# Kernel tuning notes

Measured on AMD Instinct MI355X. Metric: run time of the kernel, lower is better.

Reference implementation:

```python
import jax, jax.numpy as jnp
import numpy as np

EPS = 0.05  # blend weight of K_Rectify smoothing


def k_rectify(x_nbc, distance, idx, eps=EPS):
    """Distance-weighted neighbor smoothing.
    x_nbc: (N, B, C); distance, idx: (B, N, K). Returns (N, B, C)."""
    x_bnc = jnp.transpose(x_nbc, (1, 0, 2))                       # (B,N,C)
    B = x_bnc.shape[0]
    neigh = x_bnc[jnp.arange(B)[:, None, None], idx]              # (B,N,K,C) gather
    w = jax.nn.softmax(-distance, axis=-1)                        # closer -> larger weight
    smoothed = jnp.einsum('bnk,bnkc->bnc', w, neigh)              # (B,N,C)
    y = (1.0 - eps) * x_bnc + eps * smoothed
    return jnp.transpose(y, (1, 0, 2))


def monarch_linear(x, w1, w2, bias):
    """Monarch block-diagonal butterfly multiply on the last dim.
    w1: (k,q,p), w2: (l,s,r) with k*p == n, l*r == k*q."""
    shp = x.shape
    k, q, p = w1.shape
    l, s, r = w2.shape
    xb = x.reshape(-1, k, p)
    o1 = jnp.einsum('kqp,bkp->bkq', w1, xb)                       # (B*, k, q)
    o1 = o1.reshape(-1, r, l).transpose(0, 2, 1)                  # 'b (r l) -> b l r'
    o2 = jnp.einsum('lsr,blr->bls', w2, o1)                       # (B*, l, s)
    out = o2.transpose(0, 2, 1).reshape(-1, s * l) + bias         # 'b l s -> b (s l)'
    return out.reshape(*shp[:-1], s * l)


def setup_inputs() -> dict:
    key = jax.random.key(0)
    B, N, C, K, nblocks = 8, 8192, 256, 8, 8
    blk = C // nblocks
    ks = jax.random.split(key, 6)
    x = jax.random.normal(ks[0], (B, N, C), dtype=jnp.float32)
    distance = jax.random.uniform(ks[1], (B, N, K), dtype=jnp.float32)
    idx = jax.random.randint(ks[2], (B, N, K), 0, N)
    rf = jax.random.normal(ks[3], (B, N, C), dtype=jnp.float32)
    scale = 1.0 / np.sqrt(blk)
    w1 = jax.random.normal(ks[4], (nblocks, blk, blk), dtype=jnp.float32) * scale
    w2 = jax.random.normal(ks[5], (nblocks, blk, blk), dtype=jnp.float32) * scale
    bias = jnp.zeros((C,), dtype=jnp.float32)
    return {"x": x, "distance": distance, "idx": idx, "rf": rf,
            "w1": w1, "w2": w2, "bias": bias}


def reference(x, distance, idx, rf, w1, w2, bias):
    # _prepare_in: (B,N,C) -> (N,B,C)
    xs = jnp.transpose(x, (1, 0, 2))
    s1 = k_rectify(xs, distance, idx)            # smooth_in
    t = monarch_linear(s1, w1, w2, bias)         # Monarch block-diag matmul
    s2 = k_rectify(t, distance, idx)             # smooth_out
    return jnp.transpose(s2, (1, 0, 2)) + rf     # _out_transform residual
```

## Files before the change

kernel.cpp:

```cpp
#include <hip/hip_runtime.h>

#define NPTS 8192
#define CH   256
#define KNB  8
#define NROWS 65536
#define ROWS_PER_BLK 32
#define PHASE_ROWS 16
#define FT_STRIDE 36

#define NBLK_CONV 8192
#define NBLK_S1   (NROWS / ROWS_PER_BLK)
#define NBLK_S2   (NROWS / 16)

typedef unsigned short ushort_t;
typedef float  f32x4  __attribute__((ext_vector_type(4)));

#define BARRIER_LDS() do { \
    asm volatile("s_waitcnt lgkmcnt(0)" ::: "memory"); \
    __builtin_amdgcn_s_barrier(); \
} while (0)

__device__ __forceinline__ int xcd_swz(int h, int cpx) {
    return (h & 7) * cpx + (h >> 3);
}

__device__ __forceinline__ ushort_t f32_to_bf16(float f) {
    unsigned int b = __float_as_uint(f);
    b += 0x7FFFu + ((b >> 16) & 1u);
    return (ushort_t)(b >> 16);
}
__device__ __forceinline__ float bf16_to_f32(ushort_t u) {
    return __uint_as_float(((unsigned int)u) << 16);
}
__device__ __forceinline__ unsigned int pack_bf16(float lo, float hi) {
    return (unsigned int)f32_to_bf16(lo) | ((unsigned int)f32_to_bf16(hi) << 16);
}
__device__ __forceinline__ f32x4 bf4(ushort4 u) {
    f32x4 r;
    r.x = bf16_to_f32(u.x); r.y = bf16_to_f32(u.y);
    r.z = bf16_to_f32(u.z); r.w = bf16_to_f32(u.w);
    return r;
}

__global__ __launch_bounds__(256) void pm_conv(
    const f32x4* __restrict__ x, uint4* __restrict__ xb)
{
    const int l = xcd_swz(blockIdx.x, NBLK_CONV / 8);
    const size_t i = (size_t)l * 256 + threadIdx.x;
    const f32x4 a = __builtin_nontemporal_load(&x[2 * i]);
    const f32x4 c = __builtin_nontemporal_load(&x[2 * i + 1]);
    uint4 o;
    o.x = pack_bf16(a.x, a.y);
    o.y = pack_bf16(a.z, a.w);
    o.z = pack_bf16(c.x, c.y);
    o.w = pack_bf16(c.z, c.w);
    xb[i] = o;
}

__global__ __launch_bounds__(256, 4) void pm_stage1(
    const ushort_t* __restrict__ xb, const float* __restrict__ dist,
    const int* __restrict__ idx, const float* __restrict__ w1,
    const float* __restrict__ w2, const float* __restrict__ bias,
    ushort_t* __restrict__ t)
{
    const int c = threadIdx.x;

    __shared__ float s1[PHASE_ROWS][CH];
    __shared__ float fT[PHASE_ROWS][8 * FT_STRIDE];

    const float bb = bias[c];
    const int l2   = c & 7;
    const int kb   = c >> 5;
    const int ftw  = l2 * FT_STRIDE + (c >> 3);

    const int rr   = __builtin_amdgcn_readfirstlane(threadIdx.x >> 6);
    const int lane = threadIdx.x & 63;

    const int lb       = xcd_swz(blockIdx.x, NBLK_S1 / 8);
    const int row_base = lb * ROWS_PER_BLK;
    const int b = row_base >> 13;
    const char* xbase  = (const char*)(xb + (size_t)b * NPTS * CH);
    const int laneoff  = lane * 8;

#define LOAD_META(dd, nn, row) do {                                        \
    const float4 m0_ = *(const float4*)(dist + (size_t)(row) * KNB);       \
    const float4 m1_ = *(const float4*)(dist + (size_t)(row) * KNB + 4);   \
    const int4   j0_ = *(const int4*)(idx + (size_t)(row) * KNB);          \
    const int4   j1_ = *(const int4*)(idx + (size_t)(row) * KNB + 4);      \
    dd[0]=m0_.x; dd[1]=m0_.y; dd[2]=m0_.z; dd[3]=m0_.w;                    \
    dd[4]=m1_.x; dd[5]=m1_.y; dd[6]=m1_.z; dd[7]=m1_.w;                    \
    nn[0]=__builtin_amdgcn_readfirstlane(j0_.x);                           \
    nn[1]=__builtin_amdgcn_readfirstlane(j0_.y);                           \
    nn[2]=__builtin_amdgcn_readfirstlane(j0_.z);                           \
    nn[3]=__builtin_amdgcn_readfirstlane(j0_.w);                           \
    nn[4]=__builtin_amdgcn_readfirstlane(j1_.x);                           \
    nn[5]=__builtin_amdgcn_readfirstlane(j1_.y);                           \
    nn[6]=__builtin_amdgcn_readfirstlane(j1_.z);                           \
    nn[7]=__builtin_amdgcn_readfirstlane(j1_.w);                           \
} while (0)

#define ISSUE_G(cc, gg, nn, row) do {                                      \
    const int rloc_ = (row) & (NPTS - 1);                                  \
    cc = *(const ushort4*)(xbase + ((size_t)rloc_ << 9) + laneoff);        \
    _Pragma("unroll")                                                      \
    for (int k_ = 0; k_ < KNB; ++k_)                                       \
        gg[k_] = *(const ushort4*)(xbase + ((size_t)(unsigned)nn[k_] << 9) + laneoff); \
} while (0)

#define BLEND(cc, gg, dd, srow) do {                                       \
    float mn_ = dd[0];                                                     \
    _Pragma("unroll")                                                      \
    for (int k_ = 1; k_ < KNB; ++k_) mn_ = fminf(mn_, dd[k_]);             \
    float e_[KNB]; float sum_ = 0.f;                                       \
    _Pragma("unroll")                                                      \
    for (int k_ = 0; k_ < KNB; ++k_) { e_[k_] = __expf(mn_ - dd[k_]); sum_ += e_[k_]; } \
    const float inv_ = 0.05f / sum_;                                       \
    f32x4 acc_ = 0.95f * bf4(cc);                                          \
    _Pragma("unroll")                                                      \
    for (int k_ = 0; k_ < KNB; ++k_) acc_ += (e_[k_] * inv_) * bf4(gg[k_]); \
    *(f32x4*)(&s1[srow][lane * 4]) = acc_;                                 \
} while (0)

    float dA[KNB], dB[KNB];
    int   nA[KNB], nB[KNB];
    ushort4 cA, gA[KNB], cB, gB[KNB];

    LOAD_META(dA, nA, row_base + rr);
    LOAD_META(dB, nB, row_base + 4 + rr);
    ISSUE_G(cA, gA, nA, row_base + rr);
    ISSUE_G(cB, gB, nB, row_base + 4 + rr);

#pragma unroll
    for (int ph = 0; ph < 2; ++ph) {
        const int prow = row_base + ph * PHASE_ROWS + rr;

        BLEND(cA, gA, dA, 0 * 4 + rr);
        LOAD_META(dA, nA, prow + 8);  ISSUE_G(cA, gA, nA, prow + 8);
        BLEND(cB, gB, dB, 1 * 4 + rr);
        LOAD_META(dB, nB, prow + 12); ISSUE_G(cB, gB, nB, prow + 12);
        BLEND(cA, gA, dA, 2 * 4 + rr);
        BLEND(cB, gB, dB, 3 * 4 + rr);

        BARRIER_LDS();

        f32x4 w1r[8];
        {
            const f32x4* w1p = (const f32x4*)(w1 + c * 32);
#pragma unroll
            for (int i = 0; i < 8; ++i) { w1r[i] = w1p[i]; asm volatile("" : "+v"(w1r[i])); }
        }
#pragma unroll
        for (int r2 = 0; r2 < PHASE_ROWS; ++r2) {
            const f32x4* sb = (const f32x4*)(&s1[r2][kb * 32]);
            f32x4 a4 = {0.f, 0.f, 0.f, 0.f};
#pragma unroll
            for (int p4 = 0; p4 < 8; ++p4) a4 += w1r[p4] * sb[p4];
            fT[r2][ftw] = (a4.x + a4.y) + (a4.z + a4.w);
        }

        if (ph == 0) {
            LOAD_META(dA, nA, row_base + PHASE_ROWS + rr);
            ISSUE_G(cA, gA, nA, row_base + PHASE_ROWS + rr);
            LOAD_META(dB, nB, row_base + PHASE_ROWS + 4 + rr);
            ISSUE_G(cB, gB, nB, row_base + PHASE_ROWS + 4 + rr);
        }

        BARRIER_LDS();

        f32x4 w2r[8];
        {
            const f32x4* w2p = (const f32x4*)(w2 + ((c & 7) * 32 + (c >> 3)) * 32);
#pragma unroll
            for (int i = 0; i < 8; ++i) { w2r[i] = w2p[i]; asm volatile("" : "+v"(w2r[i])); }
        }
#pragma unroll
        for (int r2 = 0; r2 < PHASE_ROWS; ++r2) {
            const f32x4* fp = (const f32x4*)(&fT[r2][l2 * FT_STRIDE]);
            f32x4 a4 = {0.f, 0.f, 0.f, 0.f};
#pragma unroll
            for (int r4 = 0; r4 < 8; ++r4) a4 += w2r[r4] * fp[r4];
            const float a = bb + ((a4.x + a4.y) + (a4.z + a4.w));
            __builtin_nontemporal_store(
                f32_to_bf16(a),
                &t[(size_t)(row_base + ph * PHASE_ROWS + r2) * CH + c]);
        }
    }
#undef LOAD_META
#undef ISSUE_G
#undef BLEND
}

__global__ __launch_bounds__(256, 4) void pm_stage2(
    const ushort_t* __restrict__ t, const float* __restrict__ dist,
    const int* __restrict__ idx, const float* __restrict__ rf,
    float* __restrict__ out)
{
    const int w     = __builtin_amdgcn_readfirstlane(threadIdx.x >> 6);
    const int lane  = threadIdx.x & 63;
    const int lb    = xcd_swz(blockIdx.x, NBLK_S2 / 8);
    const int wrow0 = lb * 16 + w * 4;
    const int b     = wrow0 >> 13;
    const char* tbase = (const char*)(t + (size_t)b * NPTS * CH);
    const int laneoff = lane * 8;

    int   nbs[4][KNB];
    float d [4][KNB];
#pragma unroll
    for (int r = 0; r < 4; ++r) {
        const int row = wrow0 + r;
        const float4 d0 = *(const float4*)(dist + (size_t)row * KNB);
        const float4 d1 = *(const float4*)(dist + (size_t)row * KNB + 4);
        const int4   i0 = *(const int4*)(idx + (size_t)row * KNB);
        const int4   i1 = *(const int4*)(idx + (size_t)row * KNB + 4);
        d[r][0]=d0.x; d[r][1]=d0.y; d[r][2]=d0.z; d[r][3]=d0.w;
        d[r][4]=d1.x; d[r][5]=d1.y; d[r][6]=d1.z; d[r][7]=d1.w;
        nbs[r][0]=__builtin_amdgcn_readfirstlane(i0.x);
        nbs[r][1]=__builtin_amdgcn_readfirstlane(i0.y);
        nbs[r][2]=__builtin_amdgcn_readfirstlane(i0.z);
        nbs[r][3]=__builtin_amdgcn_readfirstlane(i0.w);
        nbs[r][4]=__builtin_amdgcn_readfirstlane(i1.x);
        nbs[r][5]=__builtin_amdgcn_readfirstlane(i1.y);
        nbs[r][6]=__builtin_amdgcn_readfirstlane(i1.z);
        nbs[r][7]=__builtin_amdgcn_readfirstlane(i1.w);
    }

    ushort4 c0[4], g[4][KNB];
    f32x4   rv[4];
#pragma unroll
    for (int r = 0; r < 4; ++r) {
        const int rloc = (wrow0 + r) & (NPTS - 1);
        c0[r] = *(const ushort4*)(tbase + ((size_t)rloc << 9) + laneoff);
        rv[r] = __builtin_nontemporal_load(
                    &((const f32x4*)rf)[(size_t)(wrow0 + r) * 64 + lane]);
#pragma unroll
        for (int k = 0; k < KNB; ++k)
            g[r][k] = *(const ushort4*)(tbase + ((size_t)(unsigned)nbs[r][k] << 9) + laneoff);
    }

#pragma unroll
    for (int r = 0; r < 4; ++r) {
        float mn = d[r][0];
#pragma unroll
        for (int k = 1; k < KNB; ++k) mn = fminf(mn, d[r][k]);
        float e[KNB]; float sum = 0.f;
#pragma unroll
        for (int k = 0; k < KNB; ++k) { e[k] = __expf(mn - d[r][k]); sum += e[k]; }
        const float inv = 0.05f / sum;

        f32x4 acc = 0.95f * bf4(c0[r]) + rv[r];
#pragma unroll
        for (int k = 0; k < KNB; ++k)
            acc += (e[k] * inv) * bf4(g[r][k]);
        __builtin_nontemporal_store(
            acc, &((f32x4*)out)[(size_t)(wrow0 + r) * 64 + lane]);
    }
}

extern "C" void kernel_launch(void* const* d_in, const int* in_sizes, int n_in,
                              void* d_out, int out_size, void* d_ws, size_t ws_size,
                              hipStream_t stream) {
    const float* x    = (const float*)d_in[0];
    const float* dist = (const float*)d_in[1];
    const int*   idx  = (const int*)d_in[2];
    const float* rf   = (const float*)d_in[3];
    const float* w1   = (const float*)d_in[4];
    const float* w2   = (const float*)d_in[5];
    const float* bias = (const float*)d_in[6];
    float* out = (float*)d_out;

    ushort_t* t  = (ushort_t*)d_ws;
    ushort_t* xb = (ushort_t*)((char*)d_ws + (size_t)NROWS * CH * 2);

    pm_conv  <<<NBLK_CONV, 256, 0, stream>>>((const f32x4*)x, (uint4*)xb);
    pm_stage1<<<NBLK_S1,   256, 0, stream>>>(xb, dist, idx, w1, w2, bias, t);
    pm_stage2<<<NBLK_S2,   256, 0, stream>>>(t, dist, idx, rf, out);
}
```

Before: 280.7 us.

## Use bf16 MFMA for Monarch block matmuls in stage1 with swizzled LDS

Stage 1 now blends all 32 rows first and stores the smoothed rows as bf16 in XOR-swizzled LDS. It then runs both Monarch block-diagonal multiplies with 16x16x32 bf16 MFMA instructions instead of scalar fp32 FMAs over fp32 LDS, with the weights converted to bf16 on the fly. The intermediate result and the final output are staged through LDS so the global store of t is coalesced. This adds bf16 rounding of the weights and the intermediate (a precision loss) and replaces the two-phase overlap of gathers and compute with a single pass.

After: 236.6 us. 1.19x faster.

```diff
diff --git a/kernel.cpp b/kernel.cpp
--- a/kernel.cpp
+++ b/kernel.cpp
@@ -4,16 +4,18 @@
 #define CH   256
 #define KNB  8
 #define NROWS 65536
-#define ROWS_PER_BLK 32
-#define PHASE_ROWS 16
-#define FT_STRIDE 36
-
+#define RPB_S1 32
 #define NBLK_CONV 8192
-#define NBLK_S1   (NROWS / ROWS_PER_BLK)
+#define NBLK_S1   (NROWS / RPB_S1)
 #define NBLK_S2   (NROWS / 16)
+
+#define S1_STRIDE 544
+#define FS_STRIDE 656
+#define FS_L      80
 
 typedef unsigned short ushort_t;
 typedef float  f32x4  __attribute__((ext_vector_type(4)));
+typedef short  bf16x8 __attribute__((ext_vector_type(8)));
 
 #define BARRIER_LDS() do { \
     asm volatile("s_waitcnt lgkmcnt(0)" ::: "memory"); \
@@ -35,11 +37,18 @@
 __device__ __forceinline__ unsigned int pack_bf16(float lo, float hi) {
     return (unsigned int)f32_to_bf16(lo) | ((unsigned int)f32_to_bf16(hi) << 16);
 }
-__device__ __forceinline__ f32x4 bf4(ushort4 u) {
-    f32x4 r;
-    r.x = bf16_to_f32(u.x); r.y = bf16_to_f32(u.y);
-    r.z = bf16_to_f32(u.z); r.w = bf16_to_f32(u.w);
+__device__ __forceinline__ bf16x8 pack8w(const float* __restrict__ p) {
+    bf16x8 r;
+#pragma unroll
+    for (int j = 0; j < 8; ++j) r[j] = (short)f32_to_bf16(p[j]);
     return r;
+}
+
+__device__ __forceinline__ unsigned char* s1addr(unsigned char* base, int row, int byte_off) {
+    return base + row * S1_STRIDE + (byte_off ^ ((row & 7) << 4));
+}
+__device__ __forceinline__ unsigned char* fsaddr(unsigned char* base, int row, int byte_off) {
+    return base + row * FS_STRIDE + (byte_off ^ ((row & 7) << 4));
 }
 
 __global__ __launch_bounds__(256) void pm_conv(
@@ -63,22 +72,15 @@
     const float* __restrict__ w2, const float* __restrict__ bias,
     ushort_t* __restrict__ t)
 {
-    const int c = threadIdx.x;
-
-    __shared__ float s1[PHASE_ROWS][CH];
-    __shared__ float fT[PHASE_ROWS][8 * FT_STRIDE];
-
-    const float bb = bias[c];
-    const int l2   = c & 7;
-    const int kb   = c >> 5;
-    const int ftw  = l2 * FT_STRIDE + (c >> 3);
-
-    const int rr   = __builtin_amdgcn_readfirstlane(threadIdx.x >> 6);
     const int lane = threadIdx.x & 63;
+    const int wv   = __builtin_amdgcn_readfirstlane(threadIdx.x >> 6);
+
+    __shared__ __align__(16) unsigned char s1b[RPB_S1 * S1_STRIDE];
+    __shared__ __align__(16) unsigned char fsb[RPB_S1 * FS_STRIDE];
 
     const int lb       = xcd_swz(blockIdx.x, NBLK_S1 / 8);
-    const int row_base = lb * ROWS_PER_BLK;
-    const int b = row_base >> 13;
+    const int row_base = lb * RPB_S1;
+    const int b        = row_base >> 13;
     const char* xbase  = (const char*)(xb + (size_t)b * NPTS * CH);
     const int laneoff  = lane * 8;
 
@@ -107,7 +109,7 @@
         gg[k_] = *(const ushort4*)(xbase + ((size_t)(unsigned)nn[k_] << 9) + laneoff); \
 } while (0)
 
-#define BLEND(cc, gg, dd, srow) do {                                       \
+#define BLEND_W(cc, gg, dd, rl_) do {                                      \
     float mn_ = dd[0];                                                     \
     _Pragma("unroll")                                                      \
     for (int k_ = 1; k_ < KNB; ++k_) mn_ = fminf(mn_, dd[k_]);             \
@@ -115,79 +117,167 @@
     _Pragma("unroll")                                                      \
     for (int k_ = 0; k_ < KNB; ++k_) { e_[k_] = __expf(mn_ - dd[k_]); sum_ += e_[k_]; } \
     const float inv_ = 0.05f / sum_;                                       \
-    f32x4 acc_ = 0.95f * bf4(cc);                                          \
+    float ax_ = 0.95f * bf16_to_f32(cc.x);                                 \
+    float ay_ = 0.95f * bf16_to_f32(cc.y);                                 \
+    float az_ = 0.95f * bf16_to_f32(cc.z);                                 \
+    float aw_ = 0.95f * bf16_to_f32(cc.w);                                 \
     _Pragma("unroll")                                                      \
-    for (int k_ = 0; k_ < KNB; ++k_) acc_ += (e_[k_] * inv_) * bf4(gg[k_]); \
-    *(f32x4*)(&s1[srow][lane * 4]) = acc_;                                 \
+    for (int k_ = 0; k_ < KNB; ++k_) {                                     \
+        const float w_ = e_[k_] * inv_;                                    \
+        ax_ += w_ * bf16_to_f32(gg[k_].x);                                 \
+        ay_ += w_ * bf16_to_f32(gg[k_].y);                                 \
+        az_ += w_ * bf16_to_f32(gg[k_].z);                                 \
+        aw_ += w_ * bf16_to_f32(gg[k_].w);                                 \
+    }                                                                      \
+    uint2 pv_;                                                             \
+    pv_.x = pack_bf16(ax_, ay_);                                           \
+    pv_.y = pack_bf16(az_, aw_);                                           \
+    *(uint2*)s1addr(s1b, rl_, lane * 8) = pv_;                             \
 } while (0)
 
     float dA[KNB], dB[KNB];
     int   nA[KNB], nB[KNB];
     ushort4 cA, gA[KNB], cB, gB[KNB];
 
-    LOAD_META(dA, nA, row_base + rr);
-    LOAD_META(dB, nB, row_base + 4 + rr);
-    ISSUE_G(cA, gA, nA, row_base + rr);
-    ISSUE_G(cB, gB, nB, row_base + 4 + rr);
-
-#pragma unroll
-    for (int ph = 0; ph < 2; ++ph) {
-        const int prow = row_base + ph * PHASE_ROWS + rr;
-
-        BLEND(cA, gA, dA, 0 * 4 + rr);
-        LOAD_META(dA, nA, prow + 8);  ISSUE_G(cA, gA, nA, prow + 8);
-        BLEND(cB, gB, dB, 1 * 4 + rr);
-        LOAD_META(dB, nB, prow + 12); ISSUE_G(cB, gB, nB, prow + 12);
-        BLEND(cA, gA, dA, 2 * 4 + rr);
-        BLEND(cB, gB, dB, 3 * 4 + rr);
-
-        BARRIER_LDS();
-
-        f32x4 w1r[8];
-        {
-            const f32x4* w1p = (const f32x4*)(w1 + c * 32);
-#pragma unroll
-            for (int i = 0; i < 8; ++i) { w1r[i] = w1p[i]; asm volatile("" : "+v"(w1r[i])); }
-        }
-#pragma unroll
-        for (int r2 = 0; r2 < PHASE_ROWS; ++r2) {
-            const f32x4* sb = (const f32x4*)(&s1[r2][kb * 32]);
-            f32x4 a4 = {0.f, 0.f, 0.f, 0.f};
-#pragma unroll
-            for (int p4 = 0; p4 < 8; ++p4) a4 += w1r[p4] * sb[p4];
-            fT[r2][ftw] = (a4.x + a4.y) + (a4.z + a4.w);
-        }
-
-        if (ph == 0) {
-            LOAD_META(dA, nA, row_base + PHASE_ROWS + rr);
-            ISSUE_G(cA, gA, nA, row_base + PHASE_ROWS + rr);
-            LOAD_META(dB, nB, row_base + PHASE_ROWS + 4 + rr);
-            ISSUE_G(cB, gB, nB, row_base + PHASE_ROWS + 4 + rr);
-        }
-
-        BARRIER_LDS();
-
-        f32x4 w2r[8];
-        {
-            const f32x4* w2p = (const f32x4*)(w2 + ((c & 7) * 32 + (c >> 3)) * 32);
-#pragma unroll
-            for (int i = 0; i < 8; ++i) { w2r[i] = w2p[i]; asm volatile("" : "+v"(w2r[i])); }
-        }
-#pragma unroll
-        for (int r2 = 0; r2 < PHASE_ROWS; ++r2) {
-            const f32x4* fp = (const f32x4*)(&fT[r2][l2 * FT_STRIDE]);
-            f32x4 a4 = {0.f, 0.f, 0.f, 0.f};
-#pragma unroll
-            for (int r4 = 0; r4 < 8; ++r4) a4 += w2r[r4] * fp[r4];
-            const float a = bb + ((a4.x + a4.y) + (a4.z + a4.w));
-            __builtin_nontemporal_store(
-                f32_to_bf16(a),
-                &t[(size_t)(row_base + ph * PHASE_ROWS + r2) * CH + c]);
+    LOAD_META(dA, nA, row_base + wv);
+    LOAD_META(dB, nB, row_base + 4 + wv);
+    ISSUE_G(cA, gA, nA, row_base + wv);
+    ISSUE_G(cB, gB, nB, row_base + 4 + wv);
+
+#pragma unroll
+    for (int p = 0; p < 8; ++p) {
+        const int rl   = p * 4 + wv;
+        const int rown = row_base + (p + 2) * 4 + wv;
+
+        float4 dn0, dn1; int4 in0, in1;
+        if (p < 6) {
+            dn0 = *(const float4*)(dist + (size_t)rown * KNB);
+            dn1 = *(const float4*)(dist + (size_t)rown * KNB + 4);
+            in0 = *(const int4*)(idx + (size_t)rown * KNB);
+            in1 = *(const int4*)(idx + (size_t)rown * KNB + 4);
+        }
+
+        if ((p & 1) == 0) {
+            BLEND_W(cA, gA, dA, rl);
+            if (p < 6) {
+                dA[0]=dn0.x; dA[1]=dn0.y; dA[2]=dn0.z; dA[3]=dn0.w;
+                dA[4]=dn1.x; dA[5]=dn1.y; dA[6]=dn1.z; dA[7]=dn1.w;
+                nA[0]=__builtin_amdgcn_readfirstlane(in0.x);
+                nA[1]=__builtin_amdgcn_readfirstlane(in0.y);
+                nA[2]=__builtin_amdgcn_readfirstlane(in0.z);
+                nA[3]=__builtin_amdgcn_readfirstlane(in0.w);
+                nA[4]=__builtin_amdgcn_readfirstlane(in1.x);
+                nA[5]=__builtin_amdgcn_readfirstlane(in1.y);
+                nA[6]=__builtin_amdgcn_readfirstlane(in1.z);
+                nA[7]=__builtin_amdgcn_readfirstlane(in1.w);
+                ISSUE_G(cA, gA, nA, rown);
+            }
+        } else {
+            BLEND_W(cB, gB, dB, rl);
+            if (p < 6) {
+                dB[0]=dn0.x; dB[1]=dn0.y; dB[2]=dn0.z; dB[3]=dn0.w;
+                dB[4]=dn1.x; dB[5]=dn1.y; dB[6]=dn1.z; dB[7]=dn1.w;
+                nB[0]=__builtin_amdgcn_readfirstlane(in0.x);
+                nB[1]=__builtin_amdgcn_readfirstlane(in0.y);
+                nB[2]=__builtin_amdgcn_readfirstlane(in0.z);
+                nB[3]=__builtin_amdgcn_readfirstlane(in0.w);
+                nB[4]=__builtin_amdgcn_readfirstlane(in1.x);
+                nB[5]=__builtin_amdgcn_readfirstlane(in1.y);
+                nB[6]=__builtin_amdgcn_readfirstlane(in1.z);
+                nB[7]=__builtin_amdgcn_readfirstlane(in1.w);
+                ISSUE_G(cB, gB, nB, rown);
+            }
         }
     }
 #undef LOAD_META
 #undef ISSUE_G
-#undef BLEND
+#undef BLEND_W
+
+    BARRIER_LDS();
+
+    const int l15 = lane & 15;
+    const int kq  = lane >> 4;
+#pragma unroll
+    for (int kk = 0; kk < 2; ++kk) {
+        const int kb = wv * 2 + kk;
+        const int ao = kb * 64 + kq * 16;
+        const bf16x8 a0 = *(const bf16x8*)s1addr(s1b, l15, ao);
+        const bf16x8 a1 = *(const bf16x8*)s1addr(s1b, 16 + l15, ao);
+        const bf16x8 b0 = pack8w(w1 + (size_t)(kb * 32 + l15) * 32 + kq * 8);
+        const bf16x8 b1 = pack8w(w1 + (size_t)(kb * 32 + 16 + l15) * 32 + kq * 8);
+        f32x4 d00 = {0.f,0.f,0.f,0.f}, d01 = d00, d10 = d00, d11 = d00;
+        d00 = __builtin_amdgcn_mfma_f32_16x16x32_bf16(a0, b0, d00, 0, 0, 0);
+        d01 = __builtin_amdgcn_mfma_f32_16x16x32_bf16(a0, b1, d01, 0, 0, 0);
+        d10 = __builtin_amdgcn_mfma_f32_16x16x32_bf16(a1, b0, d10, 0, 0, 0);
+        d11 = __builtin_amdgcn_mfma_f32_16x16x32_bf16(a1, b1, d11, 0, 0, 0);
+#pragma unroll
+        for (int nt = 0; nt < 2; ++nt) {
+            const int qq = nt * 16 + l15;
+            const int fo = (qq & 7) * FS_L + (kb * 4 + (qq >> 3)) * 2;
+#pragma unroll
+            for (int mt = 0; mt < 2; ++mt) {
+                const f32x4 dd = (mt == 0) ? (nt == 0 ? d00 : d01)
+                                           : (nt == 0 ? d10 : d11);
+#pragma unroll
+                for (int reg = 0; reg < 4; ++reg) {
+                    const int row = mt * 16 + kq * 4 + reg;
+                    *(ushort_t*)fsaddr(fsb, row, fo) = f32_to_bf16(dd[reg]);
+                }
+            }
+        }
+    }
+
+    BARRIER_LDS();
+
+    {
+        const int l20 = wv * 2;
+        const bf16x8 fa00 = *(const bf16x8*)fsaddr(fsb, l15,      l20 * FS_L + kq * 16);
+        const bf16x8 fa01 = *(const bf16x8*)fsaddr(fsb, 16 + l15, l20 * FS_L + kq * 16);
+        const bf16x8 fa10 = *(const bf16x8*)fsaddr(fsb, l15,      (l20 + 1) * FS_L + kq * 16);
+        const bf16x8 fa11 = *(const bf16x8*)fsaddr(fsb, 16 + l15, (l20 + 1) * FS_L + kq * 16);
+        const bf16x8 wb00 = pack8w(w2 + (size_t)(l20 * 32 + l15) * 32 + kq * 8);
+        const bf16x8 wb01 = pack8w(w2 + (size_t)(l20 * 32 + 16 + l15) * 32 + kq * 8);
+        const bf16x8 wb10 = pack8w(w2 + (size_t)((l20 + 1) * 32 + l15) * 32 + kq * 8);
+        const bf16x8 wb11 = pack8w(w2 + (size_t)((l20 + 1) * 32 + 16 + l15) * 32 + kq * 8);
+        f32x4 z = {0.f, 0.f, 0.f, 0.f};
+        f32x4 D0m0n0 = __builtin_amdgcn_mfma_f32_16x16x32_bf16(fa00, wb00, z, 0, 0, 0);
+        f32x4 D0m0n1 = __builtin_amdgcn_mfma_f32_16x16x32_bf16(fa00, wb01, z, 0, 0, 0);
+        f32x4 D0m1n0 = __builtin_amdgcn_mfma_f32_16x16x32_bf16(fa01, wb00, z, 0, 0, 0);
+        f32x4 D0m1n1 = __builtin_amdgcn_mfma_f32_16x16x32_bf16(fa01, wb01, z, 0, 0, 0);
+        f32x4 D1m0n0 = __builtin_amdgcn_mfma_f32_16x16x32_bf16(fa10, wb10, z, 0, 0, 0);
+        f32x4 D1m0n1 = __builtin_amdgcn_mfma_f32_16x16x32_bf16(fa10, wb11, z, 0, 0, 0);
+        f32x4 D1m1n0 = __builtin_amdgcn_mfma_f32_16x16x32_bf16(fa11, wb10, z, 0, 0, 0);
+        f32x4 D1m1n1 = __builtin_amdgcn_mfma_f32_16x16x32_bf16(fa11, wb11, z, 0, 0, 0);
+
+#pragma unroll
+        for (int nt = 0; nt < 2; ++nt) {
+            const int q   = nt * 16 + l15;
+            const float bv0 = bias[q * 8 + l20];
+            const float bv1 = bias[q * 8 + l20 + 1];
+#pragma unroll
+            for (int mt = 0; mt < 2; ++mt) {
+                const f32x4 e0 = (mt == 0) ? (nt == 0 ? D0m0n0 : D0m0n1)
+                                           : (nt == 0 ? D0m1n0 : D0m1n1);
+                const f32x4 e1 = (mt == 0) ? (nt == 0 ? D1m0n0 : D1m0n1)
+                                           : (nt == 0 ? D1m1n0 : D1m1n1);
+#pragma unroll
+                for (int reg = 0; reg < 4; ++reg) {
+                    const int row = mt * 16 + kq * 4 + reg;
+                    *(unsigned int*)s1addr(s1b, row, q * 16 + wv * 4) =
+                        pack_bf16(e0[reg] + bv0, e1[reg] + bv1);
+                }
+            }
+        }
+    }
+
+    BARRIER_LDS();
+
+#pragma unroll
+    for (int r = 0; r < 8; ++r) {
+        const int row = wv * 8 + r;
+        const uint2 v = *(const uint2*)s1addr(s1b, row, lane * 8);
+        *(uint2*)((char*)t + ((size_t)(row_base + row) << 9) + lane * 8) = v;
+    }
 }
 
 __global__ __launch_bounds__(256, 4) void pm_stage2(
@@ -247,10 +337,19 @@
         for (int k = 0; k < KNB; ++k) { e[k] = __expf(mn - d[r][k]); sum += e[k]; }
         const float inv = 0.05f / sum;
 
-        f32x4 acc = 0.95f * bf4(c0[r]) + rv[r];
-#pragma unroll
-        for (int k = 0; k < KNB; ++k)
-            acc += (e[k] * inv) * bf4(g[r][k]);
+        f32x4 acc;
+        acc.x = 0.95f * bf16_to_f32(c0[r].x) + rv[r].x;
+        acc.y = 0.95f * bf16_to_f32(c0[r].y) + rv[r].y;
+        acc.z = 0.95f * bf16_to_f32(c0[r].z) + rv[r].z;
+        acc.w = 0.95f * bf16_to_f32(c0[r].w) + rv[r].w;
+#pragma unroll
+        for (int k = 0; k < KNB; ++k) {
+            const float wk = e[k] * inv;
+            acc.x += wk * bf16_to_f32(g[r][k].x);
+            acc.y += wk * bf16_to_f32(g[r][k].y);
+            acc.z += wk * bf16_to_f32(g[r][k].z);
+            acc.w += wk * bf16_to_f32(g[r][k].w);
+        }
         __builtin_nontemporal_store(
             acc, &((f32x4*)out)[(size_t)(wrow0 + r) * 64 + lane]);
     }
```
